# Kernel tuning notes

Hardware: AMD Instinct MI355X
Metric: run time of the kernel (lower is better)

Reference implementation:

```python
import jax, jax.numpy as jnp
import numpy as np
import math

B, H, L, S, D = 16, 10, 4096, 77, 64
N_EMB = 20            # subject tokens per instance (positions 4..23)
SHRINK = 2.0          # subj_attn_var_shrink_factor


def setup_inputs() -> dict:
    key = jax.random.key(0)
    kq, kk, kv = jax.random.split(key, 3)
    query = jax.random.normal(kq, (B, H, L, D), dtype=jnp.float32)
    k = jax.random.normal(kk, (B, H, S, D), dtype=jnp.float32)
    v = jax.random.normal(kv, (B, H, S, D), dtype=jnp.float32)
    # instance-major subject indices: every batch instance owns tokens 4..23
    idx_b = jnp.repeat(jnp.arange(B, dtype=jnp.int32), N_EMB).reshape(B, N_EMB)
    idx_n = jnp.tile(jnp.arange(4, 4 + N_EMB, dtype=jnp.int32), (B, 1))
    return {"query": query, "key": k, "value": v, "idx_b": idx_b, "idx_n": idx_n}


def _subj_attn_scales(attn_score, idx_b, idx_n, shrink_factor):
    # attn_score: [B,H,L,S] -> permute to [B,S,H,L] as in torch code
    a2 = jnp.transpose(attn_score, (0, 3, 1, 2))
    # gather subject-token attention: [N_SUB, N_EMB, H, L]
    subj = a2[idx_b, idx_n]
    n_sub, n_emb = subj.shape[0], subj.shape[1]
    subj = subj.mean(axis=2)                       # mean over heads -> [NS,NE,L]
    prob = jax.nn.softmax(subj, axis=2)            # over spatial positions
    Hs = Ws = int(math.isqrt(L))
    p3 = prob.reshape(n_sub, n_emb, Hs, Ws)        # [NS,NE,H,W]
    ys = jnp.arange(Hs, dtype=p3.dtype).reshape(1, 1, Hs, 1)
    xs = jnp.arange(Ws, dtype=p3.dtype).reshape(1, 1, 1, Ws)
    y_c = (p3 * ys).sum(axis=(2, 3))               # [NS,NE]
    x_c = (p3 * xs).sum(axis=(2, 3))
    var_y = (p3 * ys ** 2).sum(axis=(2, 3)) - y_c ** 2
    var_x = (p3 * xs ** 2).sum(axis=(2, 3)) - x_c ** 2
    s_x = jnp.sqrt(var_x) / (shrink_factor - 1.0)
    s_y = jnp.sqrt(var_y) / (shrink_factor - 1.0)
    # torch.meshgrid default is 'ij'
    X, Y = jnp.meshgrid(jnp.arange(Ws, dtype=p3.dtype), jnp.arange(Hs, dtype=p3.dtype), indexing="ij")
    X = X[:, :, None, None]
    Y = Y[:, :, None, None]
    grid = jnp.exp(-((X - x_c) ** 2 / (2 * s_x ** 2) + (Y - y_c) ** 2 / (2 * s_y ** 2)))  # [W,H,NS,NE]
    grid = grid / jax.lax.stop_gradient(grid.max())
    grid = jnp.transpose(grid, (2, 3, 0, 1)).reshape(n_sub, n_emb, 1, L)
    # scatter back into ones: [B,S,1,L]
    scales = jnp.ones((B, S, 1, L), dtype=attn_score.dtype)
    scales = scales.at[idx_b, idx_n].set(grid)
    return jnp.transpose(scales, (0, 2, 3, 1))     # [B,1,L,S]


def reference(query, key, value, idx_b, idx_n):
    scale = 1.0 / math.sqrt(query.shape[-1])
    attn_score = jnp.einsum("bhld,bhsd->bhls", query, key) * scale  # [B,H,L,S]
    scales = _subj_attn_scales(attn_score, idx_b, idx_n, SHRINK)
    attn_w = jax.nn.softmax(attn_score, axis=-1) * scales
    out = jnp.einsum("bhls,bhsd->bhld", attn_w, value)              # [B,H,L,D]
    return out
```

## Files before the change

### kernel.cpp

```cpp
#include <hip/hip_runtime.h>
#include <math.h>

#define B_ 16
#define H_ 10
#define L_ 4096
#define S_ 77
#define D_ 64
#define NE_ 20
#define NP_ (B_*NE_)
#define SHRINK_ 2.0f
#define LOG2E 1.4426950408889634f
#define SC_L2 (0.125f*LOG2E)
#define IT_ 4

typedef __bf16 bf16x8 __attribute__((ext_vector_type(8)));
typedef float  f32x4  __attribute__((ext_vector_type(4)));

static __device__ __forceinline__ unsigned short bfb(__bf16 x) {
  return __builtin_bit_cast(unsigned short, x);
}
static __device__ __forceinline__ __bf16 mkbf(unsigned short x) {
  return __builtin_bit_cast(__bf16, x);
}

__global__ __launch_bounds__(256, 3) void k1_subj(const float* __restrict__ Q,
                                                  const float* __restrict__ K,
                                                  const int* __restrict__ idxb,
                                                  const int* __restrict__ idxn,
                                                  float* __restrict__ subj) {
  __shared__ __bf16 KF[20][2][64][8];
  __shared__ float T[NE_][66];
  __shared__ int bs[NE_], ss[NE_], s_uni;
  const int i = blockIdx.y, bx = blockIdx.x;
  const int tid = threadIdx.x, lane = tid & 63, wid = tid >> 6;
  const int c = lane & 15, g = lane >> 4;
  if (tid < NE_) { bs[tid] = idxb[i*NE_ + tid]; ss[tid] = idxn[i*NE_ + tid]; }
  __syncthreads();
  if (tid == 0) { int u = 1; for (int j = 1; j < NE_; ++j) u &= (bs[j] == bs[0]); s_uni = u; }
  for (int e4 = tid; e4 < 32*160; e4 += 256) {
    int j = e4 / 160, k = (e4 - j*160) * 4;
    float4 kv = make_float4(0.f, 0.f, 0.f, 0.f);
    if (j < NE_) kv = *(const float4*)&K[(((size_t)bs[j]*H_ + (k >> 6))*S_ + ss[j])*D_ + (k & 63)];
    int ks = k >> 5, gg = (k >> 3) & 3, jj = k & 7, n = j >> 4, cc = j & 15;
    uint2 pk;
    pk.x = (unsigned)bfb((__bf16)kv.x) | ((unsigned)bfb((__bf16)kv.y) << 16);
    pk.y = (unsigned)bfb((__bf16)kv.z) | ((unsigned)bfb((__bf16)kv.w) << 16);
    *(uint2*)&KF[ks][n][gg*16 + cc][jj] = pk;
  }
  __syncthreads();
  if (!s_uni) {
    int ll = tid & 63;
    for (int ii = 0; ii < 2; ++ii) {
      int l = bx*128 + ii*64 + ll;
      for (int j = tid >> 6; j < NE_; j += 4) {
        float a = 0.f;
        for (int h = 0; h < H_; ++h) {
          const float* qp = Q + (((size_t)bs[j]*H_ + h)*L_ + l)*D_;
          const float* kp = K + (((size_t)bs[j]*H_ + h)*S_ + ss[j])*D_;
          for (int d = 0; d < 64; ++d) a += qp[d]*kp[d];
        }
        subj[(size_t)(i*NE_ + j)*L_ + l] = a * (1.0f/80.0f);
      }
    }
    return;
  }
  const int b0 = bs[0];
  #pragma unroll 1
  for (int it = 0; it < 2; ++it) {
    const int lrow = bx*128 + it*64 + wid*16 + c;
    f32x4 acc0 = {0.f,0.f,0.f,0.f}, acc1 = {0.f,0.f,0.f,0.f};
    #pragma unroll 4
    for (int ks = 0; ks < 20; ++ks) {
      const float* qp = Q + (((size_t)b0*H_ + (ks >> 1))*L_ + lrow)*D_ + (ks & 1)*32 + g*8;
      const float4 a = *(const float4*)qp;
      const float4 bq = *(const float4*)(qp + 4);
      bf16x8 af;
      af[0]=(__bf16)a.x;  af[1]=(__bf16)a.y;  af[2]=(__bf16)a.z;  af[3]=(__bf16)a.w;
      af[4]=(__bf16)bq.x; af[5]=(__bf16)bq.y; af[6]=(__bf16)bq.z; af[7]=(__bf16)bq.w;
      bf16x8 k0 = *(bf16x8*)&KF[ks][0][lane][0];
      bf16x8 k1 = *(bf16x8*)&KF[ks][1][lane][0];
      acc0 = __builtin_amdgcn_mfma_f32_16x16x32_bf16(af, k0, acc0, 0, 0, 0);
      acc1 = __builtin_amdgcn_mfma_f32_16x16x32_bf16(af, k1, acc1, 0, 0, 0);
    }
    const float sc = 1.0f/80.0f;
    #pragma unroll
    for (int r = 0; r < 4; ++r) {
      int ll = wid*16 + g*4 + r;
      T[c][ll] = acc0[r]*sc;
      if (c < 4) T[16 + c][ll] = acc1[r]*sc;
    }
    __syncthreads();
    for (int e = tid; e < NE_*64; e += 256) {
      int j = e >> 6, ll = e & 63;
      subj[(size_t)(i*NE_ + j)*L_ + bx*128 + it*64 + ll] = T[j][ll];
    }
    __syncthreads();
  }
}

__global__ __launch_bounds__(256) void k2_moments(const float* __restrict__ subj,
                                                  float* __restrict__ params) {
  const int p = blockIdx.x;
  const int tid = threadIdx.x;
  const int lane = tid & 63, wid = tid >> 6;
  const float* sp = subj + (size_t)p*L_;
  __shared__ float red[4];
  float m = -1e30f;
  for (int l = tid; l < L_; l += 256) m = fmaxf(m, sp[l]);
  #pragma unroll
  for (int s = 1; s < 64; s <<= 1) m = fmaxf(m, __shfl_xor(m, s, 64));
  if (lane == 0) red[wid] = m;
  __syncthreads();
  m = fmaxf(fmaxf(red[0], red[1]), fmaxf(red[2], red[3]));
  __syncthreads();
  float se = 0, sy = 0, sx = 0, syy = 0, sxx = 0;
  for (int l = tid; l < L_; l += 256) {
    float e = __expf(sp[l] - m);
    float y = (float)(l >> 6), x = (float)(l & 63);
    se += e; sy += e*y; sx += e*x; syy += e*y*y; sxx += e*x*x;
  }
  float vals[5] = {se, sy, sx, syy, sxx};
  #pragma unroll
  for (int q = 0; q < 5; ++q) {
    float v = vals[q];
    #pragma unroll
    for (int s = 1; s < 64; s <<= 1) v += __shfl_xor(v, s, 64);
    if (lane == 0) red[wid] = v;
    __syncthreads();
    v = red[0] + red[1] + red[2] + red[3];
    __syncthreads();
    vals[q] = v;
  }
  if (tid == 0) {
    float xc = vals[2]/vals[0], yc = vals[1]/vals[0];
    float varx = vals[4]/vals[0] - xc*xc;
    float vary = vals[3]/vals[0] - yc*yc;
    float sh = SHRINK_ - 1.0f;
    float isx = sh*sh/(2.f*varx), isy = sh*sh/(2.f*vary);
    float rx = rintf(xc), ry = rintf(yc);
    float mv = __expf(-((rx-xc)*(rx-xc)*isx + (ry-yc)*(ry-yc)*isy));
    params[p*8+0] = xc; params[p*8+1] = yc;
    params[p*8+2] = isx; params[p*8+3] = isy; params[p*8+4] = mv;
  }
}

__global__ __launch_bounds__(256) void k2b_finish(const float* __restrict__ params,
                                                  const int* __restrict__ idxb,
                                                  const int* __restrict__ idxn,
                                                  int* __restrict__ pmap,
                                                  float* __restrict__ l2invg) {
  const int tid = threadIdx.x;
  for (int e = tid; e < B_*S_; e += 256) pmap[e] = -1;
  __syncthreads();
  for (int p = tid; p < NP_; p += 256) pmap[idxb[p]*S_ + idxn[p]] = p;
  float m = 0.f;
  for (int p = tid; p < NP_; p += 256) m = fmaxf(m, params[p*8+4]);
  #pragma unroll
  for (int s = 1; s < 64; s <<= 1) m = fmaxf(m, __shfl_xor(m, s, 64));
  __shared__ float red[4];
  if ((tid & 63) == 0) red[tid >> 6] = m;
  __syncthreads();
  if (tid == 0) {
    m = fmaxf(fmaxf(red[0], red[1]), fmaxf(red[2], red[3]));
    l2invg[0] = -log2f(m);
  }
}

__global__ __launch_bounds__(256, 1) void k3_attn(const float* __restrict__ Q,
                                                  const float* __restrict__ K,
                                                  const float* __restrict__ V,
                                                  const int* __restrict__ pmap,
                                                  const float* __restrict__ params,
                                                  const float* __restrict__ l2invg,
                                                  float* __restrict__ out) {
  __shared__ __bf16 KF[2][5][64][8];
  __shared__ __bf16 VF[3][4][64][8];
  __shared__ __bf16 Wl[4][16][104];
  __shared__ float4 pp[80];
  __shared__ float  ppc[80];

  const int bh = blockIdx.y, b = bh / H_, bx = blockIdx.x;
  const int tid = threadIdx.x, lane = tid & 63, wid = tid >> 6;
  const int c = lane & 15, g = lane >> 4;

  const float* qb0 = Q + ((size_t)bh*L_ + bx*(64*IT_) + wid*16 + c)*D_ + g*8;
  float4 nqa0 = *(const float4*)(qb0);
  float4 nqa1 = *(const float4*)(qb0 + 4);
  float4 nqc0 = *(const float4*)(qb0 + 32);
  float4 nqc1 = *(const float4*)(qb0 + 36);

  *(uint2*)&Wl[wid][c][80 + g*4] = make_uint2(0u, 0u);

  for (int e4 = tid; e4 < 80*16; e4 += 256) {
    int s = e4 >> 4, d = (e4 & 15) * 4;
    float4 kv = make_float4(0.f, 0.f, 0.f, 0.f);
    if (s < S_) kv = *(const float4*)&K[((size_t)bh*S_ + s)*D_ + d];
    int n = s >> 4, cc = s & 15, ks = d >> 5, gg = (d >> 3) & 3, jj = d & 7;
    uint2 pk;
    pk.x = (unsigned)bfb((__bf16)kv.x) | ((unsigned)bfb((__bf16)kv.y) << 16);
    pk.y = (unsigned)bfb((__bf16)kv.z) | ((unsigned)bfb((__bf16)kv.w) << 16);
    *(uint2*)&KF[ks][n][gg*16 + cc][jj] = pk;
  }
  for (int e4 = tid; e4 < 96*16; e4 += 256) {
    int s = e4 >> 4, d = (e4 & 15) * 4;
    float4 vv = make_float4(0.f, 0.f, 0.f, 0.f);
    if (s < S_) vv = *(const float4*)&V[((size_t)bh*S_ + s)*D_ + d];
    int ks = s >> 5, gg = (s >> 3) & 3, jj = s & 7;
    int n0 = d >> 4, c0 = d & 15;
    VF[ks][n0][gg*16 + c0 + 0][jj] = (__bf16)vv.x;
    VF[ks][n0][gg*16 + c0 + 1][jj] = (__bf16)vv.y;
    VF[ks][n0][gg*16 + c0 + 2][jj] = (__bf16)vv.z;
    VF[ks][n0][gg*16 + c0 + 3][jj] = (__bf16)vv.w;
  }
  for (int s = tid; s < 80; s += 256) {
    float4 v = make_float4(0.f, 0.f, 0.f, 0.f);
    float cs = 0.f;
    if (s < S_) {
      int pid = pmap[b*S_ + s];
      if (pid >= 0) {
        v.x = params[pid*8+1];
        v.y = -params[pid*8+3]*LOG2E;
        v.z = params[pid*8+0];
        v.w = -params[pid*8+2]*LOG2E;
        cs  = l2invg[0];
      }
    }
    pp[s] = v; ppc[s] = cs;
  }
  __syncthreads();

  bf16x8 kfr[2][5], vfr[3][4];
  #pragma unroll
  for (int ks = 0; ks < 2; ++ks)
    #pragma unroll
    for (int n = 0; n < 5; ++n) kfr[ks][n] = *(bf16x8*)&KF[ks][n][lane][0];
  #pragma unroll
  for (int ks = 0; ks < 3; ++ks)
    #pragma unroll
    for (int n = 0; n < 4; ++n) vfr[ks][n] = *(bf16x8*)&VF[ks][n][lane][0];

  #pragma unroll 1
  for (int it = 0; it < IT_; ++it) {
    const int lt = bx*(64*IT_) + it*64 + wid*16;
    const float4 qa0 = nqa0, qa1 = nqa1, qc0 = nqc0, qc1 = nqc1;
    {
      const int itn = (it + 1 < IT_) ? it + 1 : it;
      const float* qn = qb0 + (size_t)itn * 64 * D_;
      nqa0 = *(const float4*)(qn);
      nqa1 = *(const float4*)(qn + 4);
      nqc0 = *(const float4*)(qn + 32);
      nqc1 = *(const float4*)(qn + 36);
    }
    bf16x8 qf[2];
    qf[0][0]=(__bf16)qa0.x; qf[0][1]=(__bf16)qa0.y; qf[0][2]=(__bf16)qa0.z; qf[0][3]=(__bf16)qa0.w;
    qf[0][4]=(__bf16)qa1.x; qf[0][5]=(__bf16)qa1.y; qf[0][6]=(__bf16)qa1.z; qf[0][7]=(__bf16)qa1.w;
    qf[1][0]=(__bf16)qc0.x; qf[1][1]=(__bf16)qc0.y; qf[1][2]=(__bf16)qc0.z; qf[1][3]=(__bf16)qc0.w;
    qf[1][4]=(__bf16)qc1.x; qf[1][5]=(__bf16)qc1.y; qf[1][6]=(__bf16)qc1.z; qf[1][7]=(__bf16)qc1.w;

    f32x4 acc[5];
    #pragma unroll
    for (int n = 0; n < 5; ++n) acc[n] = f32x4{0.f, 0.f, 0.f, 0.f};
    #pragma unroll
    for (int ks = 0; ks < 2; ++ks)
      #pragma unroll
      for (int n = 0; n < 5; ++n)
        acc[n] = __builtin_amdgcn_mfma_f32_16x16x32_bf16(qf[ks], kfr[ks][n], acc[n], 0, 0, 0);
    if (c >= 13) {
      #pragma unroll
      for (int r = 0; r < 4; ++r) acc[4][r] = -1e30f;
    }
    #pragma unroll
    for (int n = 0; n < 5; ++n)
      #pragma unroll
      for (int r = 0; r < 4; ++r) acc[n][r] = __builtin_amdgcn_exp2f(acc[n][r] * SC_L2);
    float sm[4];
    #pragma unroll
    for (int r = 0; r < 4; ++r) {
      float s0 = acc[0][r] + acc[1][r] + acc[2][r] + acc[3][r] + acc[4][r];
      #pragma unroll
      for (int s = 1; s < 16; s <<= 1) s0 += __shfl_xor(s0, s, 64);
      sm[r] = __builtin_amdgcn_rcpf(s0);
    }
    const float Xf = (float)(bx*IT_ + it);
    const float Yb = (float)(wid*16 + g*4);
    #pragma unroll
    for (int n = 0; n < 5; ++n) {
      const float4 sp4 = pp[16*n + c];
      const float tx = Xf - sp4.z;
      const float Cn = fmaf(tx*tx, sp4.w, ppc[16*n + c]);
      #pragma unroll
      for (int r = 0; r < 4; ++r) {
        float t = (Yb + (float)r) - sp4.x;
        float gm = __builtin_amdgcn_exp2f(fmaf(t*t, sp4.y, Cn));
        float w = acc[n][r] * gm * sm[r];
        Wl[wid][g*4 + r][16*n + c] = (__bf16)w;
      }
    }
    f32x4 pacc[4];
    #pragma unroll
    for (int n = 0; n < 4; ++n) pacc[n] = f32x4{0.f, 0.f, 0.f, 0.f};
    #pragma unroll
    for (int ks = 0; ks < 3; ++ks) {
      bf16x8 wf = *(bf16x8*)&Wl[wid][c][ks*32 + g*8];
      #pragma unroll
      for (int n = 0; n < 4; ++n)
        pacc[n] = __builtin_amdgcn_mfma_f32_16x16x32_bf16(wf, vfr[ks][n], pacc[n], 0, 0, 0);
    }
    float* ob = out + ((size_t)bh*L_ + lt + g*4)*D_ + c;
    #pragma unroll
    for (int r = 0; r < 4; ++r)
      #pragma unroll
      for (int n = 0; n < 4; ++n) ob[(size_t)r*D_ + 16*n] = pacc[n][r];
  }
}

extern "C" void kernel_launch(void* const* d_in, const int* in_sizes, int n_in,
                              void* d_out, int out_size, void* d_ws, size_t ws_size,
                              hipStream_t stream) {
  const float* Q  = (const float*)d_in[0];
  const float* Kp = (const float*)d_in[1];
  const float* Vp = (const float*)d_in[2];
  const int* idxb = (const int*)d_in[3];
  const int* idxn = (const int*)d_in[4];
  float* out = (float*)d_out;

  char* w = (char*)d_ws;
  float* params = (float*)w;
  float* l2invg = params + NP_*8;
  int* pmap = (int*)(l2invg + 4);
  size_t head = (size_t)(NP_*8 + 4)*sizeof(float) + (size_t)B_*S_*sizeof(int);
  head = (head + 255) & ~(size_t)255;
  float* subj;
  if (ws_size >= head + (size_t)NP_*L_*sizeof(float))
    subj = (float*)(w + head);
  else
    subj = out;

  k1_subj<<<dim3(L_/128, B_), 256, 0, stream>>>(Q, Kp, idxb, idxn, subj);
  k2_moments<<<NP_, 256, 0, stream>>>(subj, params);
  k2b_finish<<<1, 256, 0, stream>>>(params, idxb, idxn, pmap, l2invg);
  k3_attn<<<dim3(L_/(64*IT_), B_*H_), 256, 0, stream>>>(Q, Kp, Vp, pmap, params, l2invg, out);
}
```

Measured before the change: 139.1 us.

## Fuse subject softmax moments into k1 via atomics and defer softmax normalization

The per-instance spatial moment reduction now runs inside k1 as exp-weighted partial sums, accumulated with atomics into a small zeroed buffer. This removes the subj intermediate buffer round-trip and the separate k2_moments launch, and k2b_finish derives centroids and variances directly. Dropping the max subtraction risks overflow for large logits, and atomic float accumulation makes the result nondeterministic. In k3, K/V fragments are read from LDS per iteration instead of held in registers, and the softmax row-sum reduction and reciprocal are moved after the PV MFMA, scaling the output instead of the weights.

```diff
diff --git a/kernel.cpp b/kernel.cpp
--- a/kernel.cpp
+++ b/kernel.cpp
@@ -27,7 +27,7 @@
                                                   const float* __restrict__ K,
                                                   const int* __restrict__ idxb,
                                                   const int* __restrict__ idxn,
-                                                  float* __restrict__ subj) {
+                                                  float* __restrict__ moments) {
   __shared__ __bf16 KF[20][2][64][8];
   __shared__ float T[NE_][66];
   __shared__ int bs[NE_], ss[NE_], s_uni;
@@ -59,12 +59,20 @@
           const float* kp = K + (((size_t)bs[j]*H_ + h)*S_ + ss[j])*D_;
           for (int d = 0; d < 64; ++d) a += qp[d]*kp[d];
         }
-        subj[(size_t)(i*NE_ + j)*L_ + l] = a * (1.0f/80.0f);
+        float e = __builtin_amdgcn_exp2f(a * (1.0f/80.0f) * LOG2E);
+        float y = (float)(l >> 6), x = (float)(l & 63);
+        atomicAdd(&moments[(i*NE_ + j)*8 + 0], e);
+        atomicAdd(&moments[(i*NE_ + j)*8 + 1], e*y);
+        atomicAdd(&moments[(i*NE_ + j)*8 + 2], e*x);
+        atomicAdd(&moments[(i*NE_ + j)*8 + 3], e*y*y);
+        atomicAdd(&moments[(i*NE_ + j)*8 + 4], e*x*x);
       }
     }
     return;
   }
   const int b0 = bs[0];
+  float mom_acc = 0.f;
+  const int rj = tid / 5, rq = tid - rj*5;
   #pragma unroll 1
   for (int it = 0; it < 2; ++it) {
     const int lrow = bx*128 + it*64 + wid*16 + c;
@@ -90,51 +98,37 @@
       if (c < 4) T[16 + c][ll] = acc1[r]*sc;
     }
     __syncthreads();
-    for (int e = tid; e < NE_*64; e += 256) {
-      int j = e >> 6, ll = e & 63;
-      subj[(size_t)(i*NE_ + j)*L_ + bx*128 + it*64 + ll] = T[j][ll];
+    if (tid < 100) {
+      const int base = bx*128 + it*64;
+      float a = 0.f;
+      for (int ll = 0; ll < 64; ++ll) {
+        float e = __builtin_amdgcn_exp2f(T[rj][ll] * LOG2E);
+        int gl = base + ll;
+        float y = (float)(gl >> 6), x = (float)(gl & 63);
+        float w = (rq == 0) ? 1.f : (rq == 1) ? y : (rq == 2) ? x
+                : (rq == 3) ? y*y : x*x;
+        a += e * w;
+      }
+      mom_acc += a;
     }
     __syncthreads();
   }
-}
-
-__global__ __launch_bounds__(256) void k2_moments(const float* __restrict__ subj,
-                                                  float* __restrict__ params) {
-  const int p = blockIdx.x;
+  if (tid < 100) atomicAdd(&moments[(i*NE_ + rj)*8 + rq], mom_acc);
+}
+
+__global__ __launch_bounds__(256) void k2b_finish(const float* __restrict__ moments,
+                                                  const int* __restrict__ idxb,
+                                                  const int* __restrict__ idxn,
+                                                  float* __restrict__ params,
+                                                  int* __restrict__ pmap,
+                                                  float* __restrict__ l2invg) {
   const int tid = threadIdx.x;
-  const int lane = tid & 63, wid = tid >> 6;
-  const float* sp = subj + (size_t)p*L_;
-  __shared__ float red[4];
-  float m = -1e30f;
-  for (int l = tid; l < L_; l += 256) m = fmaxf(m, sp[l]);
-  #pragma unroll
-  for (int s = 1; s < 64; s <<= 1) m = fmaxf(m, __shfl_xor(m, s, 64));
-  if (lane == 0) red[wid] = m;
-  __syncthreads();
-  m = fmaxf(fmaxf(red[0], red[1]), fmaxf(red[2], red[3]));
-  __syncthreads();
-  float se = 0, sy = 0, sx = 0, syy = 0, sxx = 0;
-  for (int l = tid; l < L_; l += 256) {
-    float e = __expf(sp[l] - m);
-    float y = (float)(l >> 6), x = (float)(l & 63);
-    se += e; sy += e*y; sx += e*x; syy += e*y*y; sxx += e*x*x;
-  }
-  float vals[5] = {se, sy, sx, syy, sxx};
-  #pragma unroll
-  for (int q = 0; q < 5; ++q) {
-    float v = vals[q];
-    #pragma unroll
-    for (int s = 1; s < 64; s <<= 1) v += __shfl_xor(v, s, 64);
-    if (lane == 0) red[wid] = v;
-    __syncthreads();
-    v = red[0] + red[1] + red[2] + red[3];
-    __syncthreads();
-    vals[q] = v;
-  }
-  if (tid == 0) {
-    float xc = vals[2]/vals[0], yc = vals[1]/vals[0];
-    float varx = vals[4]/vals[0] - xc*xc;
-    float vary = vals[3]/vals[0] - yc*yc;
+  for (int p = tid; p < NP_; p += 256) {
+    float m0 = moments[p*8+0], m1 = moments[p*8+1], m2 = moments[p*8+2];
+    float m3 = moments[p*8+3], m4 = moments[p*8+4];
+    float xc = m2/m0, yc = m1/m0;
+    float varx = m4/m0 - xc*xc;
+    float vary = m3/m0 - yc*yc;
     float sh = SHRINK_ - 1.0f;
     float isx = sh*sh/(2.f*varx), isy = sh*sh/(2.f*vary);
     float rx = rintf(xc), ry = rintf(yc);
@@ -142,14 +136,6 @@
     params[p*8+0] = xc; params[p*8+1] = yc;
     params[p*8+2] = isx; params[p*8+3] = isy; params[p*8+4] = mv;
   }
-}
-
-__global__ __launch_bounds__(256) void k2b_finish(const float* __restrict__ params,
-                                                  const int* __restrict__ idxb,
-                                                  const int* __restrict__ idxn,
-                                                  int* __restrict__ pmap,
-                                                  float* __restrict__ l2invg) {
-  const int tid = threadIdx.x;
   for (int e = tid; e < B_*S_; e += 256) pmap[e] = -1;
   __syncthreads();
   for (int p = tid; p < NP_; p += 256) pmap[idxb[p]*S_ + idxn[p]] = p;
@@ -229,16 +215,6 @@
   }
   __syncthreads();
 
-  bf16x8 kfr[2][5], vfr[3][4];
-  #pragma unroll
-  for (int ks = 0; ks < 2; ++ks)
-    #pragma unroll
-    for (int n = 0; n < 5; ++n) kfr[ks][n] = *(bf16x8*)&KF[ks][n][lane][0];
-  #pragma unroll
-  for (int ks = 0; ks < 3; ++ks)
-    #pragma unroll
-    for (int n = 0; n < 4; ++n) vfr[ks][n] = *(bf16x8*)&VF[ks][n][lane][0];
-
   #pragma unroll 1
   for (int it = 0; it < IT_; ++it) {
     const int lt = bx*(64*IT_) + it*64 + wid*16;
@@ -264,7 +240,7 @@
     for (int ks = 0; ks < 2; ++ks)
       #pragma unroll
       for (int n = 0; n < 5; ++n)
-        acc[n] = __builtin_amdgcn_mfma_f32_16x16x32_bf16(qf[ks], kfr[ks][n], acc[n], 0, 0, 0);
+        acc[n] = __builtin_amdgcn_mfma_f32_16x16x32_bf16(qf[ks], *(bf16x8*)&KF[ks][n][lane][0], acc[n], 0, 0, 0);
     if (c >= 13) {
       #pragma unroll
       for (int r = 0; r < 4; ++r) acc[4][r] = -1e30f;
@@ -273,14 +249,10 @@
     for (int n = 0; n < 5; ++n)
       #pragma unroll
       for (int r = 0; r < 4; ++r) acc[n][r] = __builtin_amdgcn_exp2f(acc[n][r] * SC_L2);
-    float sm[4];
-    #pragma unroll
-    for (int r = 0; r < 4; ++r) {
-      float s0 = acc[0][r] + acc[1][r] + acc[2][r] + acc[3][r] + acc[4][r];
-      #pragma unroll
-      for (int s = 1; s < 16; s <<= 1) s0 += __shfl_xor(s0, s, 64);
-      sm[r] = __builtin_amdgcn_rcpf(s0);
-    }
+    float ssum[4];
+    #pragma unroll
+    for (int r = 0; r < 4; ++r)
+      ssum[r] = acc[0][r] + acc[1][r] + acc[2][r] + acc[3][r] + acc[4][r];
     const float Xf = (float)(bx*IT_ + it);
     const float Yb = (float)(wid*16 + g*4);
     #pragma unroll
@@ -292,8 +264,7 @@
       for (int r = 0; r < 4; ++r) {
         float t = (Yb + (float)r) - sp4.x;
         float gm = __builtin_amdgcn_exp2f(fmaf(t*t, sp4.y, Cn));
-        float w = acc[n][r] * gm * sm[r];
-        Wl[wid][g*4 + r][16*n + c] = (__bf16)w;
+        Wl[wid][g*4 + r][16*n + c] = (__bf16)(acc[n][r] * gm);
       }
     }
     f32x4 pacc[4];
@@ -303,14 +274,24 @@
     for (int ks = 0; ks < 3; ++ks) {
       bf16x8 wf = *(bf16x8*)&Wl[wid][c][ks*32 + g*8];
       #pragma unroll
-      for (int n = 0; n < 4; ++n)
-        pacc[n] = __builtin_amdgcn_mfma_f32_16x16x32_bf16(wf, vfr[ks][n], pacc[n], 0, 0, 0);
+      for (int n = 0; n < 4; ++n) {
+        bf16x8 vf = *(bf16x8*)&VF[ks][n][lane][0];
+        pacc[n] = __builtin_amdgcn_mfma_f32_16x16x32_bf16(wf, vf, pacc[n], 0, 0, 0);
+      }
+    }
+    float sm[4];
+    #pragma unroll
+    for (int r = 0; r < 4; ++r) {
+      float s0 = ssum[r];
+      #pragma unroll
+      for (int s = 1; s < 16; s <<= 1) s0 += __shfl_xor(s0, s, 64);
+      sm[r] = __builtin_amdgcn_rcpf(s0);
     }
     float* ob = out + ((size_t)bh*L_ + lt + g*4)*D_ + c;
     #pragma unroll
     for (int r = 0; r < 4; ++r)
       #pragma unroll
-      for (int n = 0; n < 4; ++n) ob[(size_t)r*D_ + 16*n] = pacc[n][r];
+      for (int n = 0; n < 4; ++n) ob[(size_t)r*D_ + 16*n] = pacc[n][r] * sm[r];
   }
 }
 
@@ -325,19 +306,13 @@
   float* out = (float*)d_out;
 
   char* w = (char*)d_ws;
-  float* params = (float*)w;
-  float* l2invg = params + NP_*8;
-  int* pmap = (int*)(l2invg + 4);
-  size_t head = (size_t)(NP_*8 + 4)*sizeof(float) + (size_t)B_*S_*sizeof(int);
-  head = (head + 255) & ~(size_t)255;
-  float* subj;
-  if (ws_size >= head + (size_t)NP_*L_*sizeof(float))
-    subj = (float*)(w + head);
-  else
-    subj = out;
-
-  k1_subj<<<dim3(L_/128, B_), 256, 0, stream>>>(Q, Kp, idxb, idxn, subj);
-  k2_moments<<<NP_, 256, 0, stream>>>(subj, params);
-  k2b_finish<<<1, 256, 0, stream>>>(params, idxb, idxn, pmap, l2invg);
+  float* params  = (float*)w;
+  float* l2invg  = params + NP_*8;
+  int*   pmap    = (int*)(l2invg + 4);
+  float* moments = (float*)(pmap + B_*S_);
+
+  hipMemsetAsync(moments, 0, (size_t)NP_*8*sizeof(float), stream);
+  k1_subj<<<dim3(L_/128, B_), 256, 0, stream>>>(Q, Kp, idxb, idxn, moments);
+  k2b_finish<<<1, 256, 0, stream>>>(moments, idxb, idxn, params, pmap, l2invg);
   k3_attn<<<dim3(L_/(64*IT_), B_*H_), 256, 0, stream>>>(Q, Kp, Vp, pmap, params, l2invg, out);
 }
```

Result: slower. 148.4 us (+6.6%).
